# Performance work log

Measured on AMD Instinct MI355X. Metric: run time of the kernel, lower is better.

The kernel has to match this reference:

```python
import jax, jax.numpy as jnp
import numpy as np

HEADS = 16
DIM_HEAD = 72
RETAIN_RATE = 0.4


def setup_inputs() -> dict:
    key = jax.random.key(0)
    ks = jax.random.split(key, 6)
    B, N, D = 1, 4096, 1152
    s = D ** -0.5  # keep pre-softmax logits in a sane range
    x = jax.random.normal(ks[0], (B, N, D), dtype=jnp.float32)
    Wq = jax.random.normal(ks[1], (D, D), dtype=jnp.float32) * s
    Wk = jax.random.normal(ks[2], (D, D), dtype=jnp.float32) * s
    Wv = jax.random.normal(ks[3], (D, D), dtype=jnp.float32) * s
    Wo = jax.random.normal(ks[4], (D, D), dtype=jnp.float32) * s
    bo = jnp.zeros((D,), dtype=jnp.float32)
    return {"x": x, "Wq": Wq, "Wk": Wk, "Wv": Wv, "Wo": Wo, "bo": bo}


def reference(x, Wq, Wk, Wv, Wo, bo):
    B, N, D = x.shape
    h, dh = HEADS, DIM_HEAD
    scale = dh ** -0.5

    def split_heads(t):  # [B,N,h*dh] -> [B,h,N,dh]
        return t.reshape(B, N, h, dh).transpose(0, 2, 1, 3)

    q = split_heads(x @ Wq)
    k = split_heads(x @ Wk)
    v = split_heads(x @ Wv)

    sim = jnp.einsum("bhid,bhjd->bhij", q, k) * scale  # [B,h,N,N]
    sim = jax.nn.softmax(sim, axis=-1)

    # ---- PageRank-style power-iteration token importance (apply_wpr path) ----
    attn = sim.mean(axis=1)  # [B,N,N], mean over heads
    dist = jnp.full((B, 1, N), 1.0 / N, dtype=attn.dtype)
    for _ in range(5):  # dist @ attn^5
        dist = dist @ attn
    importance = dist.reshape(B, N)

    k_retain = int(N * RETAIN_RATE)
    _, imp_inds = jax.lax.top_k(importance, k_retain)
    _, prune_inds = jax.lax.top_k(-importance, N - k_retain)
    # torch masked-select gathers rows in ascending index order
    imp_sorted = jnp.sort(imp_inds, axis=1)        # [B, k_retain]
    prune_sorted = jnp.sort(prune_inds, axis=1)    # [B, N-k_retain]
    selected_rows = jnp.take_along_axis(attn, imp_sorted[:, :, None], axis=1)  # [B,k_retain,N]
    max_inds = jnp.argmax(selected_rows, axis=1)   # [B,N] retained-row index with max attention per column
    sim_inds = jnp.take_along_axis(max_inds, prune_sorted, axis=1)  # [B, N-k_retain]

    # ---- standard attention output ----
    out = jnp.einsum("bhij,bhjd->bhid", sim, v)    # [B,h,N,dh]
    out = out.transpose(0, 2, 1, 3).reshape(B, N, h * dh)
    out = out @ Wo + bo
    return out, importance, imp_sorted, prune_sorted, sim_inds
```

## Files before the change

kernel.cpp:

```cpp
#include <hip/hip_runtime.h>
#include <math.h>

#define NT 4096
#define DM 1152
#define NH 16
#define DH 72
#define KRET 1638
#define NPR (NT - KRET)
#define ACSB 32
#define CHUNK 205
#define SCALE 0.11785113019775793f
#define RSPLIT 2048.0f
#define INV_RSPLIT 4.8828125e-4f

typedef __attribute__((ext_vector_type(8))) short bf16x8;
typedef _Float16 f16;
typedef __attribute__((ext_vector_type(8))) _Float16 f16x8;
typedef __attribute__((ext_vector_type(4))) float f32x4;
typedef unsigned short ushort_t;

#define MFMA16(a, b, c) __builtin_amdgcn_mfma_f32_16x16x32_f16(a, b, c, 0, 0, 0)
#define MFMABF(a, b, c) __builtin_amdgcn_mfma_f32_16x16x32_bf16(a, b, c, 0, 0, 0)

__device__ inline ushort_t f2b(float f) {
    union { float f; unsigned int u; } v; v.f = f;
    unsigned int u = v.u;
    return (ushort_t)((u + 0x7FFFu + ((u >> 16) & 1u)) >> 16);
}

__device__ inline float b2f(ushort_t u) {
    union { unsigned int u; float f; } v; v.u = ((unsigned int)u) << 16;
    return v.f;
}

__device__ inline size_t qkAddr(int h, int row, int ks, int ki) {
    return ((((size_t)h * 256 + (row >> 4)) * 3 + ks) * 16 + (row & 15)) * 32 + ki;
}

__global__ __launch_bounds__(256) void split_x(
    const float* __restrict__ in, f16* __restrict__ x0, f16* __restrict__ x1,
    ushort_t* __restrict__ xb, int nElem)
{
    int i = blockIdx.x * 256 + threadIdx.x;
    int stride = gridDim.x * 256;
    for (; i < nElem; i += stride) {
        float v = in[i];
        f16 h0 = (f16)v;
        float res = (v - (float)h0) * RSPLIT;
        x0[i] = h0;
        x1[i] = (f16)res;
        xb[i] = f2b(v);
    }
}

__global__ __launch_bounds__(256) void transposeW_split(
    const float* __restrict__ W, f16* __restrict__ T0, f16* __restrict__ T1, int n)
{
    __shared__ float t[32][33];
    int bx = blockIdx.x * 32, by = blockIdx.y * 32;
    int tx = threadIdx.x & 31, ty = threadIdx.x >> 5;
    for (int i = ty; i < 32; i += 8)
        t[i][tx] = W[(size_t)(by + i) * n + bx + tx];
    __syncthreads();
    for (int i = ty; i < 32; i += 8) {
        float v = t[tx][i];
        f16 h0 = (f16)v;
        float res = (v - (float)h0) * RSPLIT;
        T0[(size_t)(bx + i) * n + by + tx] = h0;
        T1[(size_t)(bx + i) * n + by + tx] = (f16)res;
    }
}

__global__ __launch_bounds__(256) void transposeW_bf16(
    const float* __restrict__ W, ushort_t* __restrict__ WT, int n)
{
    __shared__ ushort_t t[32][33];
    int bx = blockIdx.x * 32, by = blockIdx.y * 32;
    int tx = threadIdx.x & 31, ty = threadIdx.x >> 5;
    for (int i = ty; i < 32; i += 8)
        t[i][tx] = f2b(W[(size_t)(by + i) * n + bx + tx]);
    __syncthreads();
    for (int i = ty; i < 32; i += 8)
        WT[(size_t)(bx + i) * n + by + tx] = t[tx][i];
}

__global__ __launch_bounds__(256) void proj_split3(
    const f16* __restrict__ A0, const f16* __restrict__ A1,
    const f16* __restrict__ B0, const f16* __restrict__ B1,
    f16* __restrict__ Qt0, f16* __restrict__ Qt1, float scl)
{
    __shared__ __align__(16) f16 As0[128][40];
    __shared__ __align__(16) f16 As1[128][40];
    __shared__ __align__(16) f16 Bs0[64][40];
    __shared__ __align__(16) f16 Bs1[64][40];
    const int tid = threadIdx.x;
    const int wave = tid >> 6, lane = tid & 63;
    const int r = lane & 15, g = lane >> 4;
    const int row0 = blockIdx.y * 128;
    const int col0 = blockIdx.x * 64;
    f32x4 accM[2][4] = {}, accC[2][4] = {};
    for (int k0 = 0; k0 < DM; k0 += 32) {
        for (int idx = tid; idx < 128 * 4; idx += 256) {
            int row = idx >> 2, c = idx & 3;
            size_t src = (size_t)(row0 + row) * DM + k0 + c * 8;
            *(f16x8*)&As0[row][c * 8] = *(const f16x8*)(A0 + src);
            *(f16x8*)&As1[row][c * 8] = *(const f16x8*)(A1 + src);
        }
        for (int idx = tid; idx < 64 * 4; idx += 256) {
            int row = idx >> 2, c = idx & 3;
            size_t src = (size_t)(col0 + row) * DM + k0 + c * 8;
            *(f16x8*)&Bs0[row][c * 8] = *(const f16x8*)(B0 + src);
            *(f16x8*)&Bs1[row][c * 8] = *(const f16x8*)(B1 + src);
        }
        __syncthreads();
        f16x8 a0[2], a1[2], b0[4], b1[4];
#pragma unroll
        for (int rf = 0; rf < 2; ++rf) {
            a0[rf] = *(const f16x8*)&As0[wave * 32 + rf * 16 + r][g * 8];
            a1[rf] = *(const f16x8*)&As1[wave * 32 + rf * 16 + r][g * 8];
        }
#pragma unroll
        for (int cf = 0; cf < 4; ++cf) {
            b0[cf] = *(const f16x8*)&Bs0[cf * 16 + r][g * 8];
            b1[cf] = *(const f16x8*)&Bs1[cf * 16 + r][g * 8];
        }
#pragma unroll
        for (int rf = 0; rf < 2; ++rf)
#pragma unroll
            for (int cf = 0; cf < 4; ++cf) {
                accM[rf][cf] = MFMA16(a0[rf], b0[cf], accM[rf][cf]);
                accC[rf][cf] = MFMA16(a0[rf], b1[cf], accC[rf][cf]);
                accC[rf][cf] = MFMA16(a1[rf], b0[cf], accC[rf][cf]);
            }
        __syncthreads();
    }
#pragma unroll
    for (int rf = 0; rf < 2; ++rf)
#pragma unroll
        for (int cf = 0; cf < 4; ++cf) {
            int col = col0 + cf * 16 + r;
            int head = col / DH;
            int c = col - head * DH;
            int ks = c >> 5, ki = c & 31;
#pragma unroll
            for (int j = 0; j < 4; ++j) {
                int row = row0 + wave * 32 + rf * 16 + g * 4 + j;
                float v = (accM[rf][cf][j] + accC[rf][cf][j] * INV_RSPLIT) * scl;
                f16 h0 = (f16)v;
                float res = (v - (float)h0) * RSPLIT;
                size_t addr = qkAddr(head, row, ks, ki);
                Qt0[addr] = h0;
                Qt1[addr] = (f16)res;
            }
        }
}

__global__ __launch_bounds__(256) void gemm_bf16_lds(
    const ushort_t* __restrict__ A, const ushort_t* __restrict__ BT,
    const float* __restrict__ bias, void* __restrict__ C, int mode,
    int Nn, int K)
{
    __shared__ __align__(16) ushort_t As[128][40];
    __shared__ __align__(16) ushort_t Bs[64][40];
    const int tid = threadIdx.x;
    const int wave = tid >> 6, lane = tid & 63;
    const int r = lane & 15, g = lane >> 4;
    const int row0 = blockIdx.y * 128;
    const int col0 = blockIdx.x * 64;
    f32x4 acc[2][4] = {};
    for (int k0 = 0; k0 < K; k0 += 32) {
        for (int idx = tid; idx < 128 * 4; idx += 256) {
            int row = idx >> 2, c = idx & 3;
            *(bf16x8*)&As[row][c * 8] = *(const bf16x8*)(A + (size_t)(row0 + row) * K + k0 + c * 8);
        }
        for (int idx = tid; idx < 64 * 4; idx += 256) {
            int row = idx >> 2, c = idx & 3;
            *(bf16x8*)&Bs[row][c * 8] = *(const bf16x8*)(BT + (size_t)(col0 + row) * K + k0 + c * 8);
        }
        __syncthreads();
        bf16x8 a[2], b[4];
#pragma unroll
        for (int rf = 0; rf < 2; ++rf)
            a[rf] = *(const bf16x8*)&As[wave * 32 + rf * 16 + r][g * 8];
#pragma unroll
        for (int cf = 0; cf < 4; ++cf)
            b[cf] = *(const bf16x8*)&Bs[cf * 16 + r][g * 8];
#pragma unroll
        for (int rf = 0; rf < 2; ++rf)
#pragma unroll
            for (int cf = 0; cf < 4; ++cf)
                acc[rf][cf] = MFMABF(a[rf], b[cf], acc[rf][cf]);
        __syncthreads();
    }
#pragma unroll
    for (int rf = 0; rf < 2; ++rf)
#pragma unroll
        for (int cf = 0; cf < 4; ++cf) {
            int col = col0 + cf * 16 + r;
            float bv = bias ? bias[col] : 0.f;
#pragma unroll
            for (int j = 0; j < 4; ++j) {
                int row = row0 + wave * 32 + rf * 16 + g * 4 + j;
                float vv = acc[rf][cf][j] + bv;
                if (mode == 2) {
                    int head = col / DH;
                    int d = col - head * DH;
                    size_t addr = (((size_t)head * 128 + (row >> 5)) * 80 + d) * 32 + (row & 31);
                    ((ushort_t*)C)[addr] = f2b(vv);
                } else {
                    ((float*)C)[(size_t)row * Nn + col] = vv;
                }
            }
        }
}

__global__ __launch_bounds__(256) void rowsum_pv(
    const f16* __restrict__ Qt0, const f16* __restrict__ Qt1,
    const f16* __restrict__ Kt0, const f16* __restrict__ Kt1,
    const ushort_t* __restrict__ Vp,
    float* __restrict__ rsPart, ushort_t* __restrict__ part_pv)
{
    __shared__ __align__(16) f16 KL[2][6144];
    const int tid = threadIdx.x;
    const int wv = tid >> 6, lane = tid & 63;
    const int r = lane & 15, g = lane >> 4;
    const int h = blockIdx.y;
    const int half = blockIdx.z;
    const int rowblk = blockIdx.x * 4 + wv;
    f16x8 a0[3], a1[3];
#pragma unroll
    for (int ks = 0; ks < 3; ++ks) {
        size_t o = ((((size_t)h * 256 + rowblk) * 3 + ks) * 16) * 32 + r * 32 + g * 8;
        a0[ks] = *(const f16x8*)(Qt0 + o);
        a1[ks] = *(const f16x8*)(Qt1 + o);
    }
    const int c32p0 = ((r >> 2) << 3) + (r & 3);
    float rs = 0.f;
    f32x4 oacc[5] = {};
    for (int ct = half * 32; ct < half * 32 + 32; ++ct) {
        __syncthreads();
        const size_t ctBase = ((size_t)h * 256 + ct * 4) * 1536;
#pragma unroll
        for (int s = 0; s < 6; ++s) {
            int wc = s * 4 + wv;
            int plane = wc >= 12;
            int cip = wc - plane * 12;
            const f16* src = (plane ? Kt1 : Kt0) + ctBase + cip * 512 + lane * 8;
            *(f16x8*)&KL[plane][cip * 512 + lane * 8] = *(const f16x8*)src;
        }
        __syncthreads();
        f32x4 accM[4] = {}, accC[4] = {};
#pragma unroll
        for (int ks = 0; ks < 3; ++ks) {
#pragma unroll
            for (int group = 0; group < 2; ++group) {
#pragma unroll
                for (int cfp = 0; cfp < 2; ++cfp) {
                    const int c32 = c32p0 + cfp * 4;
                    const int off = (((group * 2 + (c32 >> 4)) * 3 + ks) << 9)
                                  + ((c32 & 15) << 5) + (g << 3);
                    f16x8 b0 = *(const f16x8*)&KL[0][off];
                    f16x8 b1 = *(const f16x8*)&KL[1][off];
                    const int cf = group * 2 + cfp;
                    accM[cf] = MFMA16(b0, a0[ks], accM[cf]);
                    accC[cf] = MFMA16(b1, a0[ks], accC[cf]);
                    accC[cf] = MFMA16(b0, a1[ks], accC[cf]);
                }
            }
        }
        const int kt0 = ct * 2;
#pragma unroll
        for (int group = 0; group < 2; ++group) {
            bf16x8 pa;
#pragma unroll
            for (int cfp = 0; cfp < 2; ++cfp) {
                const int cf = group * 2 + cfp;
#pragma unroll
                for (int j = 0; j < 4; ++j) {
                    float ev = __expf(accM[cf][j] + accC[cf][j] * INV_RSPLIT);
                    rs += ev;
                    pa[cfp * 4 + j] = (short)f2b(ev);
                }
            }
#pragma unroll
            for (int t = 0; t < 5; ++t) {
                int col = t * 16 + r;
                size_t vo = (((size_t)h * 128 + kt0 + group) * 80 + col) * 32 + g * 8;
                bf16x8 b = *(const bf16x8*)(Vp + vo);
                oacc[t] = MFMABF(pa, b, oacc[t]);
            }
        }
    }
    rs += __shfl_xor(rs, 16);
    rs += __shfl_xor(rs, 32);
    if (g == 0)
        rsPart[((size_t)half * NH + h) * NT + rowblk * 16 + r] = rs;
#pragma unroll
    for (int t = 0; t < 5; ++t) {
        int col = t * 16 + r;
        if (col < DH) {
#pragma unroll
            for (int j = 0; j < 4; ++j) {
                int row = rowblk * 16 + g * 4 + j;
                part_pv[(((size_t)half * NH + h) * NT + row) * DH + col] = f2b(oacc[t][j]);
            }
        }
    }
}

__global__ __launch_bounds__(256) void pv_norm(
    const float* __restrict__ rsPart, const ushort_t* __restrict__ part_pv,
    float* __restrict__ invs, ushort_t* __restrict__ otmpb)
{
    __shared__ float sinv[32];
    const int h = blockIdx.x;
    const int row0 = blockIdx.y * 32;
    const int tid = threadIdx.x;
    if (tid < 32) {
        float rsA = rsPart[(size_t)h * NT + row0 + tid];
        float rsB = rsPart[((size_t)NH + h) * NT + row0 + tid];
        float inv = 1.0f / (rsA + rsB);
        sinv[tid] = inv;
        invs[(size_t)h * NT + row0 + tid] = inv;
    }
    __syncthreads();
    for (int e = tid; e < 32 * DH; e += 256) {
        int rr = e / DH, col = e - rr * DH;
        int row = row0 + rr;
        float a = b2f(part_pv[((size_t)h * NT + row) * DH + col]);
        float b = b2f(part_pv[(((size_t)NH + h) * NT + row) * DH + col]);
        otmpb[(size_t)row * DM + h * DH + col] = f2b((a + b) * sinv[rr]);
    }
}

__global__ __launch_bounds__(256) void attn_sum(
    const f16* __restrict__ Qt0, const f16* __restrict__ Qt1,
    const f16* __restrict__ Kt0, const f16* __restrict__ Kt1,
    const float* __restrict__ invs, float* __restrict__ attn)
{
    __shared__ __align__(16) f16 KL[2][6144];
    const int tid = threadIdx.x;
    const int wr = tid >> 6, lane = tid & 63;
    const int r = lane & 15, g = lane >> 4;
    const int cs = blockIdx.x;
    const int rowblk = blockIdx.y * 4 + wr;
    const int row0 = rowblk * 16;
    const int cb0 = cs * 8;
    float aacc[2][4][4] = {};
    for (int h = 0; h < NH; ++h) {
        f16x8 a0[3], a1[3];
#pragma unroll
        for (int ks = 0; ks < 3; ++ks) {
            size_t o = ((((size_t)h * 256 + rowblk) * 3 + ks) * 16) * 32 + r * 32 + g * 8;
            a0[ks] = *(const f16x8*)(Qt0 + o);
            a1[ks] = *(const f16x8*)(Qt1 + o);
        }
        float vinv[4];
#pragma unroll
        for (int j = 0; j < 4; ++j)
            vinv[j] = invs[(size_t)h * NT + row0 + g * 4 + j];
#pragma unroll
        for (int ct = 0; ct < 2; ++ct) {
            __syncthreads();
            const size_t ctBase = ((size_t)h * 256 + cb0 + ct * 4) * 1536;
#pragma unroll
            for (int s = 0; s < 6; ++s) {
                int wc = s * 4 + wr;
                int plane = wc >= 12;
                int cip = wc - plane * 12;
                const f16* src = (plane ? Kt1 : Kt0) + ctBase + cip * 512 + lane * 8;
                *(f16x8*)&KL[plane][cip * 512 + lane * 8] = *(const f16x8*)src;
            }
            __syncthreads();
            f32x4 accM[4] = {}, accC[4] = {};
#pragma unroll
            for (int ks = 0; ks < 3; ++ks) {
#pragma unroll
                for (int cf = 0; cf < 4; ++cf) {
                    f16x8 b0 = *(const f16x8*)&KL[0][(cf * 3 + ks) * 512 + r * 32 + g * 8];
                    f16x8 b1 = *(const f16x8*)&KL[1][(cf * 3 + ks) * 512 + r * 32 + g * 8];
                    accM[cf] = MFMA16(a0[ks], b0, accM[cf]);
                    accC[cf] = MFMA16(a0[ks], b1, accC[cf]);
                    accC[cf] = MFMA16(a1[ks], b0, accC[cf]);
                }
            }
#pragma unroll
            for (int cf = 0; cf < 4; ++cf) {
#pragma unroll
                for (int j = 0; j < 4; ++j) {
                    float p = __expf(accM[cf][j] + accC[cf][j] * INV_RSPLIT) * vinv[j];
                    aacc[ct][cf][j] += p;
                }
            }
        }
    }
#pragma unroll
    for (int ct = 0; ct < 2; ++ct) {
        const int colbase = cs * 128 + ct * 64;
#pragma unroll
        for (int cf = 0; cf < 4; ++cf) {
#pragma unroll
            for (int j = 0; j < 4; ++j) {
                int row = row0 + g * 4 + j;
                attn[(size_t)row * NT + colbase + cf * 16 + r] = aacc[ct][cf][j] * 0.0625f;
            }
        }
    }
}

__global__ __launch_bounds__(256) void init_dist(float* __restrict__ d)
{
    int t = blockIdx.x * 256 + threadIdx.x;
    if (t < NT) d[t] = 1.0f / NT;
}

__global__ __launch_bounds__(256) void power_a(
    const float* __restrict__ attn, const float* __restrict__ din,
    float* __restrict__ part)
{
    int j = blockIdx.x * 256 + threadIdx.x;
    int i0 = blockIdx.y * 128;
    float acc = 0.f;
    for (int i = i0; i < i0 + 128; ++i)
        acc += din[i] * attn[(size_t)i * NT + j];
    part[(size_t)blockIdx.y * NT + j] = acc;
}

__global__ __launch_bounds__(256) void power_b(
    const float* __restrict__ part, float* __restrict__ dout)
{
    int j = blockIdx.x * 256 + threadIdx.x;
    float acc = 0.f;
    for (int ib = 0; ib < 32; ++ib) acc += part[(size_t)ib * NT + j];
    dout[j] = acc;
}

__global__ __launch_bounds__(256) void rank_count(
    const float* __restrict__ imp, int* __restrict__ rank, int* __restrict__ prank)
{
    __shared__ float sj[256];
    const int tid = threadIdx.x;
    const int jb = blockIdx.y * 256;
    sj[tid] = imp[jb + tid];
    __syncthreads();
    const int i = blockIdx.x * 256 + tid;
    const float mv = imp[i];
    int r = 0, rp = 0;
    for (int jj = 0; jj < 256; ++jj) {
        float vj = sj[jj];
        int j = jb + jj;
        int tie_low = (vj == mv) && (j < i);
        r  += (vj > mv) || tie_low;
        rp += (vj < mv) || tie_low;
    }
    atomicAdd(&rank[i], r);
    atomicAdd(&prank[i], rp);
}

__global__ __launch_bounds__(256) void scatter_topk2(
    const int* __restrict__ rank, const int* __restrict__ prank,
    float* __restrict__ out_imps, float* __restrict__ out_prune,
    int* __restrict__ imp_rows, int* __restrict__ prune_cols)
{
    __shared__ unsigned char fr[NT];
    __shared__ unsigned char fp[NT];
    __shared__ int sr[256], sp[256];
    const int tid = threadIdx.x;
    for (int t = tid; t < NT; t += 256) {
        fr[t] = rank[t] < KRET;
        fp[t] = prank[t] < NPR;
    }
    __syncthreads();
    const int base = tid * 16;
    int cr = 0, cp = 0;
#pragma unroll
    for (int e = 0; e < 16; ++e) { cr += fr[base + e]; cp += fp[base + e]; }
    sr[tid] = cr; sp[tid] = cp;
    __syncthreads();
    int pr = 0, pp = 0;
    for (int j = 0; j < tid; ++j) { pr += sr[j]; pp += sp[j]; }
#pragma unroll
    for (int e = 0; e < 16; ++e) {
        int i = base + e;
        if (fr[i]) { out_imps[pr] = (float)i; imp_rows[pr] = i; ++pr; }
        if (fp[i]) { out_prune[pp] = (float)i; prune_cols[pp] = i; ++pp; }
    }
}

__global__ __launch_bounds__(256) void argmax_part(
    const float* __restrict__ attn, const int* __restrict__ imp_rows,
    float* __restrict__ pbest, int* __restrict__ pbi)
{
    __shared__ int rows[CHUNK];
    const int tid = threadIdx.x;
    const int rc = blockIdx.y;
    const int r0 = rc * CHUNK;
    const int nr = min(KRET - r0, CHUNK);
    for (int t = tid; t < nr; t += 256) rows[t] = imp_rows[r0 + t];
    __syncthreads();
    const int j = blockIdx.x * 256 + tid;
    float best = -INFINITY;
    int bi = 0;
    for (int rr = 0; rr < nr; ++rr) {
        float val = attn[(size_t)rows[rr] * NT + j];
        if (val > best) { best = val; bi = r0 + rr; }
    }
    pbest[(size_t)rc * NT + j] = best;
    pbi[(size_t)rc * NT + j] = bi;
}

__global__ __launch_bounds__(256) void argmax_red(
    const float* __restrict__ pbest, const int* __restrict__ pbi,
    int* __restrict__ maxind)
{
    const int j = blockIdx.x * 256 + threadIdx.x;
    float best = -INFINITY;
    int bi = 0;
#pragma unroll
    for (int rc = 0; rc < 8; ++rc) {
        float val = pbest[(size_t)rc * NT + j];
        if (val > best) { best = val; bi = pbi[(size_t)rc * NT + j]; }
    }
    maxind[j] = bi;
}

__global__ __launch_bounds__(256) void finalize(
    const float* __restrict__ dist, const int* __restrict__ prune_cols,
    const int* __restrict__ maxind, float* __restrict__ out_imp,
    float* __restrict__ out_simi)
{
    int t = blockIdx.x * 256 + threadIdx.x;
    if (t < NT) out_imp[t] = dist[t];
    if (t < NPR) out_simi[t] = (float)maxind[prune_cols[t]];
}

extern "C" void kernel_launch(void* const* d_in, const int* in_sizes, int n_in,
                              void* d_out, int out_size, void* d_ws, size_t ws_size,
                              hipStream_t stream)
{
    const float* x  = (const float*)d_in[0];
    const float* Wq = (const float*)d_in[1];
    const float* Wk = (const float*)d_in[2];
    const float* Wv = (const float*)d_in[3];
    const float* Wo = (const float*)d_in[4];
    const float* bo = (const float*)d_in[5];
    float* out = (float*)d_out;

    const size_t QKT_EL = (size_t)NH * 256 * 3 * 16 * 32;
    const size_t VP_EL  = (size_t)NH * 128 * 80 * 32;

    float* ws = (float*)d_ws;
    size_t off = 0;
    float* attn = ws + off; off += (size_t)NT * NT;
    f16* Qt0 = (f16*)(ws + off); off += QKT_EL / 2;
    f16* Qt1 = (f16*)(ws + off); off += QKT_EL / 2;
    f16* Kt0 = (f16*)(ws + off); off += QKT_EL / 2;
    f16* Kt1 = (f16*)(ws + off); off += QKT_EL / 2;
    ushort_t* Vp = (ushort_t*)(ws + off); off += VP_EL / 2;
    size_t zero_floats = 4 * (QKT_EL / 2) + VP_EL / 2;
    ushort_t* otmpb = (ushort_t*)(ws + off); off += ((size_t)NT * DM) / 2;
    f16* X0 = (f16*)(ws + off); f16* X1 = X0 + (size_t)NT * DM; off += (size_t)NT * DM;
    f16* T0 = (f16*)(ws + off); f16* T1 = T0 + (size_t)DM * DM; off += (size_t)DM * DM;
    ushort_t* Wslot = (ushort_t*)(ws + off); off += ((size_t)DM * DM) / 2;
    float* invs    = ws + off; off += (size_t)NH * NT;
    float* rsPart  = ws + off; off += (size_t)2 * NH * NT;
    ushort_t* part_pv = (ushort_t*)(ws + off); off += (size_t)2 * NH * NT * DH / 2;
    float* pbest   = ws + off; off += 8 * NT;
    int*   pbi     = (int*)(ws + off); off += 8 * NT;
    float* dist0 = ws + off; off += NT;
    float* dist1 = ws + off; off += NT;
    float* partial = ws + off; off += 32 * NT;
    int* rank      = (int*)(ws + off); off += NT;
    int* prank     = (int*)(ws + off); off += NT;
    int* imp_rows  = (int*)(ws + off); off += 2048;
    int* prune_cols= (int*)(ws + off); off += 2560;
    int* maxind    = (int*)(ws + off); off += NT;

    ushort_t* xb = (ushort_t*)attn;

    float* out_out   = out;
    float* out_imp   = out + (size_t)NT * DM;
    float* out_imps  = out_imp + NT;
    float* out_prune = out_imps + KRET;
    float* out_simi  = out_prune + NPR;

    hipMemsetAsync(Qt0, 0, zero_floats * sizeof(float), stream);
    split_x<<<2048, 256, 0, stream>>>(x, X0, X1, xb, NT * DM);

    dim3 gT(DM / 32, DM / 32);
    dim3 gP(DM / 64, NT / 128);
    transposeW_split<<<gT, 256, 0, stream>>>(Wq, T0, T1, DM);
    proj_split3<<<gP, 256, 0, stream>>>(X0, X1, T0, T1, Qt0, Qt1, SCALE);
    transposeW_split<<<gT, 256, 0, stream>>>(Wk, T0, T1, DM);
    proj_split3<<<gP, 256, 0, stream>>>(X0, X1, T0, T1, Kt0, Kt1, 1.0f);

    transposeW_bf16<<<gT, 256, 0, stream>>>(Wv, Wslot, DM);
    gemm_bf16_lds<<<gP, 256, 0, stream>>>(xb, Wslot, nullptr, Vp, 2, DM, DM);

    rowsum_pv<<<dim3(NT / 64, NH, 2), 256, 0, stream>>>(Qt0, Qt1, Kt0, Kt1, Vp,
                                                        rsPart, part_pv);
    pv_norm<<<dim3(NH, NT / 32), 256, 0, stream>>>(rsPart, part_pv, invs, otmpb);

    attn_sum<<<dim3(ACSB, NT / 64), 256, 0, stream>>>(Qt0, Qt1, Kt0, Kt1, invs, attn);

    transposeW_bf16<<<gT, 256, 0, stream>>>(Wo, Wslot, DM);
    gemm_bf16_lds<<<gP, 256, 0, stream>>>(otmpb, Wslot, bo, out_out, 0, DM, DM);

    init_dist<<<16, 256, 0, stream>>>(dist0);
    float* da = dist0;
    float* db = dist1;
    for (int it = 0; it < 5; ++it) {
        power_a<<<dim3(16, 32), 256, 0, stream>>>(attn, da, partial);
        power_b<<<16, 256, 0, stream>>>(partial, db);
        float* t = da; da = db; db = t;
    }

    hipMemsetAsync(rank, 0, 2 * NT * sizeof(int), stream);
    rank_count<<<dim3(16, 16), 256, 0, stream>>>(da, rank, prank);
    scatter_topk2<<<1, 256, 0, stream>>>(rank, prank, out_imps, out_prune,
                                         imp_rows, prune_cols);
    argmax_part<<<dim3(16, 8), 256, 0, stream>>>(attn, imp_rows, pbest, pbi);
    argmax_red<<<16, 256, 0, stream>>>(pbest, pbi, maxind);
    finalize<<<16, 256, 0, stream>>>(da, prune_cols, maxind, out_imp, out_simi);
}
```

Before: 843.3 us.

## Split rowsum_pv key range four ways, halve attn_sum column tile, pack bf16 conversion

rowsum_pv now splits the key dimension into four partitions instead of two, and pv_norm sums four partials. attn_sum gives each block 64 columns instead of 128, doubling its grid to expose more parallelism and cut register use. Exp values are packed to bf16 with the v_cvt_pk_bf16_f32 instruction instead of manual rounding. The partial buffers are aliased onto the attn and X workspace to save memory, which depends on those buffers being dead at that point in the stream and adds more partial traffic.

Measured after the change: 837.8 us. Within noise of the previous version (-0.7%).

```diff
diff --git a/kernel.cpp b/kernel.cpp
--- a/kernel.cpp
+++ b/kernel.cpp
@@ -7,7 +7,8 @@
 #define DH 72
 #define KRET 1638
 #define NPR (NT - KRET)
-#define ACSB 32
+#define QSPLIT 4
+#define ACSB 64
 #define CHUNK 205
 #define SCALE 0.11785113019775793f
 #define RSPLIT 2048.0f
@@ -225,7 +226,7 @@
     const int wv = tid >> 6, lane = tid & 63;
     const int r = lane & 15, g = lane >> 4;
     const int h = blockIdx.y;
-    const int half = blockIdx.z;
+    const int quar = blockIdx.z;
     const int rowblk = blockIdx.x * 4 + wv;
     f16x8 a0[3], a1[3];
 #pragma unroll
@@ -237,7 +238,7 @@
     const int c32p0 = ((r >> 2) << 3) + (r & 3);
     float rs = 0.f;
     f32x4 oacc[5] = {};
-    for (int ct = half * 32; ct < half * 32 + 32; ++ct) {
+    for (int ct = quar * 16; ct < quar * 16 + 16; ++ct) {
         __syncthreads();
         const size_t ctBase = ((size_t)h * 256 + ct * 4) * 1536;
 #pragma unroll
@@ -271,7 +272,7 @@
         const int kt0 = ct * 2;
 #pragma unroll
         for (int group = 0; group < 2; ++group) {
-            bf16x8 pa;
+            float e[8];
 #pragma unroll
             for (int cfp = 0; cfp < 2; ++cfp) {
                 const int cf = group * 2 + cfp;
@@ -279,22 +280,30 @@
                 for (int j = 0; j < 4; ++j) {
                     float ev = __expf(accM[cf][j] + accC[cf][j] * INV_RSPLIT);
                     rs += ev;
-                    pa[cfp * 4 + j] = (short)f2b(ev);
+                    e[cfp * 4 + j] = ev;
                 }
+            }
+            union { bf16x8 v; unsigned w[4]; } pa;
+#pragma unroll
+            for (int wi = 0; wi < 4; ++wi) {
+                unsigned rw;
+                asm("v_cvt_pk_bf16_f32 %0, %1, %2"
+                    : "=v"(rw) : "v"(e[wi * 2]), "v"(e[wi * 2 + 1]));
+                pa.w[wi] = rw;
             }
 #pragma unroll
             for (int t = 0; t < 5; ++t) {
                 int col = t * 16 + r;
                 size_t vo = (((size_t)h * 128 + kt0 + group) * 80 + col) * 32 + g * 8;
                 bf16x8 b = *(const bf16x8*)(Vp + vo);
-                oacc[t] = MFMABF(pa, b, oacc[t]);
+                oacc[t] = MFMABF(pa.v, b, oacc[t]);
             }
         }
     }
     rs += __shfl_xor(rs, 16);
     rs += __shfl_xor(rs, 32);
     if (g == 0)
-        rsPart[((size_t)half * NH + h) * NT + rowblk * 16 + r] = rs;
+        rsPart[((size_t)quar * NH + h) * NT + rowblk * 16 + r] = rs;
 #pragma unroll
     for (int t = 0; t < 5; ++t) {
         int col = t * 16 + r;
@@ -302,7 +311,7 @@
 #pragma unroll
             for (int j = 0; j < 4; ++j) {
                 int row = rowblk * 16 + g * 4 + j;
-                part_pv[(((size_t)half * NH + h) * NT + row) * DH + col] = f2b(oacc[t][j]);
+                part_pv[(((size_t)quar * NH + h) * NT + row) * DH + col] = f2b(oacc[t][j]);
             }
         }
     }
@@ -317,9 +326,11 @@
     const int row0 = blockIdx.y * 32;
     const int tid = threadIdx.x;
     if (tid < 32) {
-        float rsA = rsPart[(size_t)h * NT + row0 + tid];
-        float rsB = rsPart[((size_t)NH + h) * NT + row0 + tid];
-        float inv = 1.0f / (rsA + rsB);
+        float s = 0.f;
+#pragma unroll
+        for (int q = 0; q < QSPLIT; ++q)
+            s += rsPart[((size_t)q * NH + h) * NT + row0 + tid];
+        float inv = 1.0f / s;
         sinv[tid] = inv;
         invs[(size_t)h * NT + row0 + tid] = inv;
     }
@@ -327,9 +338,11 @@
     for (int e = tid; e < 32 * DH; e += 256) {
         int rr = e / DH, col = e - rr * DH;
         int row = row0 + rr;
-        float a = b2f(part_pv[((size_t)h * NT + row) * DH + col]);
-        float b = b2f(part_pv[(((size_t)NH + h) * NT + row) * DH + col]);
-        otmpb[(size_t)row * DM + h * DH + col] = f2b((a + b) * sinv[rr]);
+        float s = 0.f;
+#pragma unroll
+        for (int q = 0; q < QSPLIT; ++q)
+            s += b2f(part_pv[(((size_t)q * NH + h) * NT + row) * DH + col]);
+        otmpb[(size_t)row * DM + h * DH + col] = f2b(s * sinv[rr]);
     }
 }
 
@@ -345,8 +358,8 @@
     const int cs = blockIdx.x;
     const int rowblk = blockIdx.y * 4 + wr;
     const int row0 = rowblk * 16;
-    const int cb0 = cs * 8;
-    float aacc[2][4][4] = {};
+    const int cb0 = cs * 4;
+    float aacc[4][4] = {};
     for (int h = 0; h < NH; ++h) {
         f16x8 a0[3], a1[3];
 #pragma unroll
@@ -359,51 +372,45 @@
 #pragma unroll
         for (int j = 0; j < 4; ++j)
             vinv[j] = invs[(size_t)h * NT + row0 + g * 4 + j];
-#pragma unroll
-        for (int ct = 0; ct < 2; ++ct) {
-            __syncthreads();
-            const size_t ctBase = ((size_t)h * 256 + cb0 + ct * 4) * 1536;
-#pragma unroll
-            for (int s = 0; s < 6; ++s) {
-                int wc = s * 4 + wr;
-                int plane = wc >= 12;
-                int cip = wc - plane * 12;
-                const f16* src = (plane ? Kt1 : Kt0) + ctBase + cip * 512 + lane * 8;
-                *(f16x8*)&KL[plane][cip * 512 + lane * 8] = *(const f16x8*)src;
-            }
-            __syncthreads();
-            f32x4 accM[4] = {}, accC[4] = {};
-#pragma unroll
-            for (int ks = 0; ks < 3; ++ks) {
-#pragma unroll
-                for (int cf = 0; cf < 4; ++cf) {
-                    f16x8 b0 = *(const f16x8*)&KL[0][(cf * 3 + ks) * 512 + r * 32 + g * 8];
-                    f16x8 b1 = *(const f16x8*)&KL[1][(cf * 3 + ks) * 512 + r * 32 + g * 8];
-                    accM[cf] = MFMA16(a0[ks], b0, accM[cf]);
-                    accC[cf] = MFMA16(a0[ks], b1, accC[cf]);
-                    accC[cf] = MFMA16(a1[ks], b0, accC[cf]);
-                }
-            }
+        __syncthreads();
+        const size_t ctBase = ((size_t)h * 256 + cb0) * 1536;
+#pragma unroll
+        for (int s = 0; s < 6; ++s) {
+            int wc = s * 4 + wr;
+            int plane = wc >= 12;
+            int cip = wc - plane * 12;
+            const f16* src = (plane ? Kt1 : Kt0) + ctBase + cip * 512 + lane * 8;
+            *(f16x8*)&KL[plane][cip * 512 + lane * 8] = *(const f16x8*)src;
+        }
+        __syncthreads();
+        f32x4 accM[4] = {}, accC[4] = {};
+#pragma unroll
+        for (int ks = 0; ks < 3; ++ks) {
 #pragma unroll
             for (int cf = 0; cf < 4; ++cf) {
-#pragma unroll
-                for (int j = 0; j < 4; ++j) {
-                    float p = __expf(accM[cf][j] + accC[cf][j] * INV_RSPLIT) * vinv[j];
-                    aacc[ct][cf][j] += p;
-                }
-            }
-        }
-    }
-#pragma unroll
-    for (int ct = 0; ct < 2; ++ct) {
-        const int colbase = cs * 128 + ct * 64;
+                f16x8 b0 = *(const f16x8*)&KL[0][(cf * 3 + ks) * 512 + r * 32 + g * 8];
+                f16x8 b1 = *(const f16x8*)&KL[1][(cf * 3 + ks) * 512 + r * 32 + g * 8];
+                accM[cf] = MFMA16(a0[ks], b0, accM[cf]);
+                accC[cf] = MFMA16(a0[ks], b1, accC[cf]);
+                accC[cf] = MFMA16(a1[ks], b0, accC[cf]);
+            }
+        }
 #pragma unroll
         for (int cf = 0; cf < 4; ++cf) {
 #pragma unroll
             for (int j = 0; j < 4; ++j) {
-                int row = row0 + g * 4 + j;
-                attn[(size_t)row * NT + colbase + cf * 16 + r] = aacc[ct][cf][j] * 0.0625f;
-            }
+                float p = __expf(accM[cf][j] + accC[cf][j] * INV_RSPLIT) * vinv[j];
+                aacc[cf][j] += p;
+            }
+        }
+    }
+    const int colbase = cs * 64;
+#pragma unroll
+    for (int cf = 0; cf < 4; ++cf) {
+#pragma unroll
+        for (int j = 0; j < 4; ++j) {
+            int row = row0 + g * 4 + j;
+            attn[(size_t)row * NT + colbase + cf * 16 + r] = aacc[cf][j] * 0.0625f;
         }
     }
 }
@@ -559,12 +566,11 @@
     ushort_t* Vp = (ushort_t*)(ws + off); off += VP_EL / 2;
     size_t zero_floats = 4 * (QKT_EL / 2) + VP_EL / 2;
     ushort_t* otmpb = (ushort_t*)(ws + off); off += ((size_t)NT * DM) / 2;
-    f16* X0 = (f16*)(ws + off); f16* X1 = X0 + (size_t)NT * DM; off += (size_t)NT * DM;
+    f16* X0 = (f16*)(ws + off); f16* X1 = X0 + (size_t)NT * DM;
+    float* xs_base = ws + off; off += (size_t)NT * DM;
     f16* T0 = (f16*)(ws + off); f16* T1 = T0 + (size_t)DM * DM; off += (size_t)DM * DM;
     ushort_t* Wslot = (ushort_t*)(ws + off); off += ((size_t)DM * DM) / 2;
     float* invs    = ws + off; off += (size_t)NH * NT;
-    float* rsPart  = ws + off; off += (size_t)2 * NH * NT;
-    ushort_t* part_pv = (ushort_t*)(ws + off); off += (size_t)2 * NH * NT * DH / 2;
     float* pbest   = ws + off; off += 8 * NT;
     int*   pbi     = (int*)(ws + off); off += 8 * NT;
     float* dist0 = ws + off; off += NT;
@@ -577,6 +583,8 @@
     int* maxind    = (int*)(ws + off); off += NT;
 
     ushort_t* xb = (ushort_t*)attn;
+    ushort_t* part_pv = (ushort_t*)attn;
+    float* rsPart = xs_base;
 
     float* out_out   = out;
     float* out_imp   = out + (size_t)NT * DM;
@@ -597,8 +605,8 @@
     transposeW_bf16<<<gT, 256, 0, stream>>>(Wv, Wslot, DM);
     gemm_bf16_lds<<<gP, 256, 0, stream>>>(xb, Wslot, nullptr, Vp, 2, DM, DM);
 
-    rowsum_pv<<<dim3(NT / 64, NH, 2), 256, 0, stream>>>(Qt0, Qt1, Kt0, Kt1, Vp,
-                                                        rsPart, part_pv);
+    rowsum_pv<<<dim3(NT / 64, NH, QSPLIT), 256, 0, stream>>>(Qt0, Qt1, Kt0, Kt1, Vp,
+                                                             rsPart, part_pv);
     pv_norm<<<dim3(NH, NT / 32), 256, 0, stream>>>(rsPart, part_pv, invs, otmpb);
 
     attn_sum<<<dim3(ACSB, NT / 64), 256, 0, stream>>>(Qt0, Qt1, Kt0, Kt1, invs, attn);
```
